# Kernel tuning notes

Hardware: AMD Instinct MI355X
Metric: run time of the kernel (lower is better)

Reference implementation:

```python
import jax, jax.numpy as jnp
import numpy as np
from jax import lax

RATIOS = (0.5, 1.0, 2.0)
SCALES = (8, 16, 32)
BASE = 16
STRIDE = 16
NMS_THRESH = 0.7
N_PRE = 6000   # n_test_pre_nms
N_POST = 300   # n_test_post_nms
MIN_SIZE = 16.0  # min_size * scale (scale=1.0)
NEG = -1e9


def _anchor_base():
    py = px = BASE / 2.0
    ab = np.zeros((len(RATIOS) * len(SCALES), 4), np.float32)
    for i, r in enumerate(RATIOS):
        for j, s in enumerate(SCALES):
            h = BASE * s * np.sqrt(r)
            w = BASE * s * np.sqrt(1.0 / r)
            k = i * len(SCALES) + j
            ab[k] = [py - h / 2.0, px - w / 2.0, py + h / 2.0, px + w / 2.0]
    return ab


def _anchors(hh, ww):
    # enumerate shifted anchors, shape [hh*ww*9, 4] in (y1,x1,y2,x2)
    ab = _anchor_base()
    sy = np.arange(hh, dtype=np.float32) * STRIDE
    sx = np.arange(ww, dtype=np.float32) * STRIDE
    sx, sy = np.meshgrid(sx, sy)
    shift = np.stack([sy.ravel(), sx.ravel(), sy.ravel(), sx.ravel()], axis=1)
    a = (ab[None, :, :] + shift[:, None, :]).reshape(-1, 4).astype(np.float32)
    return jnp.asarray(a)


def _conv(x, w, b, pad):
    y = lax.conv_general_dilated(x, w, (1, 1), [(pad, pad), (pad, pad)],
                                 dimension_numbers=('NCHW', 'OIHW', 'NCHW'))
    return y + b[None, :, None, None]


def _nms(boxes, valid):
    # greedy NMS over score-sorted boxes [N,4]; returns N_POST selected indices (-1 = pad)
    N = boxes.shape[0]
    y1, x1, y2, x2 = boxes[:, 0], boxes[:, 1], boxes[:, 2], boxes[:, 3]
    area = (y2 - y1) * (x2 - x1)
    idx = jnp.arange(N)

    def body(i, sup):
        cur = valid[i] & (~sup[i])
        ih = jnp.clip(jnp.minimum(y2[i], y2) - jnp.maximum(y1[i], y1), 0.0)
        iw = jnp.clip(jnp.minimum(x2[i], x2) - jnp.maximum(x1[i], x1), 0.0)
        inter = ih * iw
        iou = inter / (area[i] + area - inter + 1e-9)
        return sup | (cur & (iou > NMS_THRESH) & (idx > i))

    sup = lax.fori_loop(0, N, body, jnp.zeros((N,), bool))
    kept = valid & (~sup)
    rank = jnp.cumsum(kept) - 1
    sel = jnp.full((N_POST,), -1, jnp.int32)
    sel = sel.at[jnp.where(kept & (rank < N_POST), rank, N_POST)].set(
        jnp.arange(N, dtype=jnp.int32), mode='drop')
    return sel


def setup_inputs() -> dict:
    key = jax.random.key(0)
    ks = jax.random.split(key, 5)
    n, c, hh, ww = 8, 512, 64, 64
    x = jax.random.normal(ks[0], (n, c, hh, ww), jnp.float32)
    # normal_init(mean=0, std=0.01), biases zero
    w1 = 0.01 * jax.random.normal(ks[1], (512, 512, 3, 3), jnp.float32)
    b1 = jnp.zeros((512,), jnp.float32)
    w_score = 0.01 * jax.random.normal(ks[2], (18, 512, 1, 1), jnp.float32)
    b_score = jnp.zeros((18,), jnp.float32)
    w_loc = 0.01 * jax.random.normal(ks[3], (36, 512, 1, 1), jnp.float32)
    b_loc = jnp.zeros((36,), jnp.float32)
    return {"x": x, "w1": w1, "b1": b1, "w_score": w_score, "b_score": b_score,
            "w_loc": w_loc, "b_loc": b_loc, "img_h": 1024, "img_w": 1024}


def reference(x, w1, b1, w_score, b_score, w_loc, b_loc, img_h, img_w):
    n, _, hh, ww = x.shape
    anchor = _anchors(hh, ww)  # [K,4]
    mid = jax.nn.relu(_conv(x, w1, b1, 1))
    rpn_locs = _conv(mid, w_loc, b_loc, 0).transpose(0, 2, 3, 1).reshape(n, -1, 4)  # [n,K,4]
    raw = _conv(mid, w_score, b_score, 0).transpose(0, 2, 3, 1)  # [n,hh,ww,18]
    sm = jax.nn.softmax(raw.reshape(n, hh, ww, -1, 2), axis=-1)
    fg = sm[..., 1].reshape(n, -1)          # [n,K] foreground scores
    rpn_scores = raw.reshape(n, -1, 2)      # pre-softmax, as in original
    # loc2bbox decode
    ah = anchor[:, 2] - anchor[:, 0]
    aw = anchor[:, 3] - anchor[:, 1]
    acy = anchor[:, 0] + 0.5 * ah
    acx = anchor[:, 1] + 0.5 * aw
    dy, dx, dh, dw = (rpn_locs[..., 0], rpn_locs[..., 1], rpn_locs[..., 2], rpn_locs[..., 3])
    cy = dy * ah + acy
    cx = dx * aw + acx
    h = ah * jnp.exp(dh)
    w = aw * jnp.exp(dw)
    fh = jnp.float32(img_h)
    fw = jnp.float32(img_w)
    roi = jnp.stack([jnp.clip(cy - 0.5 * h, 0.0, fh), jnp.clip(cx - 0.5 * w, 0.0, fw),
                     jnp.clip(cy + 0.5 * h, 0.0, fh), jnp.clip(cx + 0.5 * w, 0.0, fw)], axis=-1)
    hs = roi[..., 2] - roi[..., 0]
    ws = roi[..., 3] - roi[..., 1]
    ok = (hs >= MIN_SIZE) & (ws >= MIN_SIZE)
    masked = jnp.where(ok, fg, NEG)
    vals, top = lax.top_k(masked, N_PRE)  # score-descending pre-NMS selection
    boxes = jnp.take_along_axis(roi, top[..., None], axis=1)  # [n,N_PRE,4]
    valid = vals > NEG / 2
    sel = jax.vmap(_nms)(boxes, valid)  # [n,N_POST]
    mask = sel >= 0
    rois = jnp.take_along_axis(boxes, jnp.clip(sel, 0)[..., None], axis=1)
    rois = jnp.where(mask[..., None], rois, 0.0)  # [n,N_POST,4], zero-padded
    roi_indices = jnp.where(mask, jnp.arange(n, dtype=jnp.int32)[:, None], -1)  # -1 = pad
    return (rpn_locs, rpn_scores, rois, roi_indices, anchor)
```

## Files before the change

kernel.cpp:

```cpp
#include <hip/hip_runtime.h>
#include <cstdint>
#include <cstddef>

#define CIN 512
#define NA 36864
#define NPRE 6000
#define NPOST 300
#define NWORD 94
#define NEGV -1000000000.0f
#define ISTRIDE 76

#define O_LOCS   0
#define O_SCORES 1179648
#define O_ROIS   1769472
#define O_RIDX   1779072
#define O_ANCH   1781472

__device__ __forceinline__ float fmulr(float a, float b) { return __fmul_rn(a, b); }
__device__ __forceinline__ float faddr(float a, float b) { return __fadd_rn(a, b); }
__device__ __forceinline__ float fsubr(float a, float b) { return __fsub_rn(a, b); }

__device__ __forceinline__ void anchor_for(int a, int pos, float* anc) {
    const double rat[3] = {0.5, 1.0, 2.0};
    const double scl[3] = {8.0, 16.0, 32.0};
    int ri = a / 3, si = a - ri * 3;
    double h = 16.0 * scl[si] * sqrt(rat[ri]);
    double w = 16.0 * scl[si] * sqrt(1.0 / rat[ri]);
    float a0 = (float)(8.0 - h * 0.5);
    float a1 = (float)(8.0 - w * 0.5);
    float a2 = (float)(8.0 + h * 0.5);
    float a3 = (float)(8.0 + w * 0.5);
    int y = pos >> 6, x = pos & 63;
    float sy = (float)(y * 16), sx = (float)(x * 16);
    anc[0] = faddr(a0, sy); anc[1] = faddr(a1, sx);
    anc[2] = faddr(a2, sy); anc[3] = faddr(a3, sx);
}

__device__ __forceinline__ bool decode_box(float4 L, const float* anc, float* box) {
    float ah  = fsubr(anc[2], anc[0]);
    float aw  = fsubr(anc[3], anc[1]);
    float acy = faddr(anc[0], fmulr(0.5f, ah));
    float acx = faddr(anc[1], fmulr(0.5f, aw));
    float cy  = faddr(fmulr(L.x, ah), acy);
    float cx  = faddr(fmulr(L.y, aw), acx);
    float h   = fmulr(ah, expf(L.z));
    float w   = fmulr(aw, expf(L.w));
    float y1 = fminf(fmaxf(fsubr(cy, fmulr(0.5f, h)), 0.0f), 1024.0f);
    float x1 = fminf(fmaxf(fsubr(cx, fmulr(0.5f, w)), 0.0f), 1024.0f);
    float y2 = fminf(fmaxf(faddr(cy, fmulr(0.5f, h)), 0.0f), 1024.0f);
    float x2 = fminf(fmaxf(faddr(cx, fmulr(0.5f, w)), 0.0f), 1024.0f);
    box[0] = y1; box[1] = x1; box[2] = y2; box[3] = x2;
    float hs = fsubr(y2, y1), ws2 = fsubr(x2, x1);
    return (hs >= 16.0f) && (ws2 >= 16.0f);
}

__device__ __forceinline__ unsigned long long mono64(double f) {
    unsigned long long u = (unsigned long long)__double_as_longlong(f);
    return (u & 0x8000000000000000ull) ? ~u : (u | 0x8000000000000000ull);
}

__global__ __launch_bounds__(256) void k_wreord(const float* __restrict__ w1,
                                                float* __restrict__ wr2) {
    __shared__ float tile[64][37];
    const int ct0 = blockIdx.x * 36;
    const int ocb = blockIdx.y;
    const int t = threadIdx.x;
    for (int i = t; i < 64 * 36; i += 256) {
        int orow = i / 36, c = i - orow * 36;
        tile[orow][c] = w1[(size_t)(ocb * 64 + orow) * 4608 + ct0 + c];
    }
    __syncthreads();
    for (int i = t; i < 36 * 64; i += 256) {
        int ct = i >> 6, o = i & 63;
        wr2[((size_t)ocb * 4608 + ct0 + ct) * 64 + o] = tile[o][ct];
    }
}

__global__ __launch_bounds__(256, 2) void k_conv3(const float* __restrict__ x,
                                                  const float* __restrict__ wr2,
                                                  const float* __restrict__ b1,
                                                  float* __restrict__ mid) {
    __shared__ float in_s[8 * 6 * ISTRIDE];
    __shared__ float w_s[8 * 9 * 64];
    const int yb  = blockIdx.x;
    const int ocb = blockIdx.y;
    const int n   = blockIdx.z;
    const int t   = threadIdx.x;
    const int y0  = yb * 4;
    const int cg  = t & 7;
    const int rg  = (t >> 3) & 1;
    const int ocg = t >> 4;
    const int xo  = cg << 3;

    if (t < 48) { in_s[t * ISTRIDE + 4] = 0.f; in_s[t * ISTRIDE + 69] = 0.f; }

    int   ilds[3];
    int   ival[3];
    const float* igp[3];
#pragma unroll
    for (int k = 0; k < 3; ++k) {
        int s = t + k * 256;
        int row = s >> 4, c = s & 15;
        int cc = row / 6, rr = row - cc * 6;
        int gy = y0 - 1 + rr;
        ival[k] = (gy >= 0 && gy < 64) ? 1 : 0;
        int gyc = min(max(gy, 0), 63);
        ilds[k] = row * ISTRIDE + 5 + c * 4;
        igp[k]  = x + (((size_t)(n * CIN + cc) * 64 + gyc) * 64 + c * 4);
    }
    const float* wgp = wr2 + (size_t)ocb * (4608 * 64);

    float acc[4][2][8];
#pragma unroll
    for (int o = 0; o < 4; o++)
#pragma unroll
        for (int rr = 0; rr < 2; rr++)
#pragma unroll
            for (int j = 0; j < 8; j++) acc[o][rr][j] = 0.f;

    for (int ch = 0; ch < 64; ++ch) {
        const float* wp0 = wgp + (size_t)ch * 4608;
#pragma unroll
        for (int k = 0; k < 4; ++k)
            *(float4*)&w_s[4 * t + 1024 * k] = *(const float4*)(wp0 + 4 * t + 1024 * k);
        if (t < 128)
            *(float4*)&w_s[4 * t + 4096] = *(const float4*)(wp0 + 4 * t + 4096);
#pragma unroll
        for (int k = 0; k < 3; ++k) {
            float4 v = make_float4(0.f, 0.f, 0.f, 0.f);
            if (ival[k]) v = *(const float4*)(igp[k] + (size_t)ch * 32768);
            in_s[ilds[k] + 0] = v.x;
            in_s[ilds[k] + 1] = v.y;
            in_s[ilds[k] + 2] = v.z;
            in_s[ilds[k] + 3] = v.w;
        }
        __syncthreads();

        float sub[4][2][8];
#pragma unroll
        for (int o = 0; o < 4; o++)
#pragma unroll
            for (int rr = 0; rr < 2; rr++)
#pragma unroll
                for (int j = 0; j < 8; j++) sub[o][rr][j] = 0.f;
#pragma unroll 1
        for (int cc = 0; cc < 8; ++cc) {
            float in4r[4][12];
#pragma unroll
            for (int k = 0; k < 4; ++k) {
                const float4* ip = (const float4*)
                    &in_s[cc * (6 * ISTRIDE) + (rg * 2 + k) * ISTRIDE + xo + 4];
                float4 A = ip[0], B = ip[1], C4 = ip[2];
                in4r[k][0] = A.x;  in4r[k][1] = A.y;  in4r[k][2]  = A.z;  in4r[k][3]  = A.w;
                in4r[k][4] = B.x;  in4r[k][5] = B.y;  in4r[k][6]  = B.z;  in4r[k][7]  = B.w;
                in4r[k][8] = C4.x; in4r[k][9] = C4.y; in4r[k][10] = C4.z; in4r[k][11] = C4.w;
            }
#pragma unroll
            for (int dy = 0; dy < 3; ++dy) {
#pragma unroll
                for (int dx = 0; dx < 3; ++dx) {
                    const float4* wp =
                        (const float4*)&w_s[cc * 576 + (dy * 3 + dx) * 64 + ocg * 4];
                    float4 W = wp[0];
                    float w4[4] = {W.x, W.y, W.z, W.w};
#pragma unroll
                    for (int o = 0; o < 4; ++o)
#pragma unroll
                        for (int rr = 0; rr < 2; ++rr)
#pragma unroll
                            for (int j = 0; j < 8; ++j)
                                sub[o][rr][j] += w4[o] * in4r[rr + dy][j + dx];
                }
            }
        }
#pragma unroll
        for (int o = 0; o < 4; o++)
#pragma unroll
            for (int rr = 0; rr < 2; rr++)
#pragma unroll
                for (int j = 0; j < 8; j++) acc[o][rr][j] += sub[o][rr][j];
        __syncthreads();
    }
    const int ocbase = (ocb << 6) + ocg * 4;
#pragma unroll
    for (int o = 0; o < 4; o++) {
        float bb = b1[ocbase + o];
#pragma unroll
        for (int rr = 0; rr < 2; rr++) {
            const int gy = y0 + rg * 2 + rr;
            float4 v0, v1;
            v0.x = fmaxf(acc[o][rr][0] + bb, 0.f);
            v0.y = fmaxf(acc[o][rr][1] + bb, 0.f);
            v0.z = fmaxf(acc[o][rr][2] + bb, 0.f);
            v0.w = fmaxf(acc[o][rr][3] + bb, 0.f);
            v1.x = fmaxf(acc[o][rr][4] + bb, 0.f);
            v1.y = fmaxf(acc[o][rr][5] + bb, 0.f);
            v1.z = fmaxf(acc[o][rr][6] + bb, 0.f);
            v1.w = fmaxf(acc[o][rr][7] + bb, 0.f);
            float* mp = &mid[((size_t)(n * CIN + ocbase + o) * 64 + gy) * 64 + xo];
            *(float4*)(mp + 0) = v0;
            *(float4*)(mp + 4) = v1;
        }
    }
}

__global__ __launch_bounds__(256) void k_conv1(const float* __restrict__ mid,
                                               const float* __restrict__ wl,
                                               const float* __restrict__ bl,
                                               const float* __restrict__ wsc,
                                               const float* __restrict__ bs,
                                               float* __restrict__ out,
                                               double* __restrict__ fgbuf) {
    __shared__ float in_s[128 * 64];
    __shared__ float w_s[128 * 64];
    const int y = blockIdx.x;
    const int n = blockIdx.y;
    const int t = threadIdx.x;
    const int xx = t & 63, og = t >> 6;
    double accd[14];
#pragma unroll
    for (int k = 0; k < 14; k++) accd[k] = 0.0;

    for (int c0 = 0; c0 < 512; c0 += 128) {
        for (int idx = t; idx < 128 * 64; idx += 256) {
            int cc = idx >> 6, x2 = idx & 63;
            in_s[idx] = mid[((n * CIN + c0 + cc) * 64 + y) * 64 + x2];
        }
        for (int idx = t; idx < 128 * 64; idx += 256) {
            int cc = idx >> 6, s = idx & 63;
            int og2 = s >> 4, kk = s & 15;
            int oc = og2 * 14 + kk;
            float v = 0.f;
            if (kk < 14 && oc < 54)
                v = (oc < 36) ? wl[oc * 512 + c0 + cc] : wsc[(oc - 36) * 512 + c0 + cc];
            w_s[cc * 64 + s] = v;
        }
        __syncthreads();
#pragma unroll 1
        for (int cc = 0; cc < 128; ++cc) {
            double iv = (double)in_s[cc * 64 + xx];
            const float4* wq = (const float4*)&w_s[cc * 64 + og * 16];
            float4 W0 = wq[0], W1 = wq[1], W2 = wq[2], W3 = wq[3];
            float wf[16] = {W0.x, W0.y, W0.z, W0.w, W1.x, W1.y, W1.z, W1.w,
                            W2.x, W2.y, W2.z, W2.w, W3.x, W3.y, W3.z, W3.w};
#pragma unroll
            for (int k = 0; k < 14; k++)
                accd[k] += (double)wf[k] * iv;
        }
        __syncthreads();
    }
    const int pos = y * 64 + xx;
    double sv[14];
#pragma unroll
    for (int k = 0; k < 14; k++) {
        int oc = og * 14 + k;
        if (oc >= 54) break;
        if (oc < 36) {
            double v = accd[k] + (double)bl[oc];
            int a = oc >> 2, cd = oc & 3;
            out[O_LOCS + ((size_t)(n * NA + pos * 9 + a)) * 4 + cd] = (float)v;
        } else {
            sv[k] = accd[k] + (double)bs[oc - 36];
            int c2 = oc - 36, a = c2 >> 1, cls = c2 & 1;
            out[O_SCORES + ((size_t)(n * NA + pos * 9 + a)) * 2 + cls] = (float)sv[k];
        }
    }
#pragma unroll
    for (int k = 0; k < 13; k++) {
        int oc = og * 14 + k;
        if (oc >= 36 && oc < 54 && ((oc - 36) & 1) == 0) {
            double s0 = sv[k], s1 = sv[k + 1];
            double m = fmax(s0, s1);
            double e0 = exp(s0 - m), e1 = exp(s1 - m);
            double fg = e1 / (e0 + e1);
            int a = (oc - 36) >> 1;
            fgbuf[(size_t)n * NA + pos * 9 + a] = fg;
        }
    }
}

__global__ __launch_bounds__(256) void k_keys(const float* __restrict__ out_ro,
                                              const double* __restrict__ fgbuf,
                                              unsigned long long* __restrict__ keys,
                                              float* __restrict__ out) {
    const int n = blockIdx.x / 144;
    const int i = (blockIdx.x % 144) * 256 + threadIdx.x;
    int pos = i / 9, a = i - pos * 9;
    float anc[4]; anchor_for(a, pos, anc);
    float4 L = *(const float4*)&out_ro[O_LOCS + (size_t)(n * NA + i) * 4];
    float box[4];
    bool ok = decode_box(L, anc, box);
    double f = ok ? fgbuf[(size_t)n * NA + i] : (double)NEGV;
    unsigned long long m = mono64(f);
    keys[(size_t)n * NA + i] =
        (m & 0xFFFFFFFFFFFF0000ull) | (unsigned long long)(0xFFFFu - (unsigned)i);
    if (blockIdx.x < 144) {
        out[O_ANCH + (size_t)i * 4 + 0] = anc[0];
        out[O_ANCH + (size_t)i * 4 + 1] = anc[1];
        out[O_ANCH + (size_t)i * 4 + 2] = anc[2];
        out[O_ANCH + (size_t)i * 4 + 3] = anc[3];
    }
}

__global__ __launch_bounds__(1024) void k_select(const unsigned long long* __restrict__ keys,
                                                 unsigned long long* __restrict__ kth,
                                                 unsigned int* __restrict__ cnt) {
    __shared__ unsigned int hist[8192];
    __shared__ unsigned int gs[256];
    __shared__ unsigned int s_rem, s_G;
    __shared__ unsigned long long s_pref;
    const int n = blockIdx.x, t = threadIdx.x;
    if (t == 0) { s_rem = NPRE; s_pref = 0ull; }
    __syncthreads();
    const int shifts[5] = {51, 38, 25, 12, 0};
    const int widths[5] = {13, 13, 13, 13, 12};
    int plen = 0;
    for (int lev = 0; lev < 5; ++lev) {
        const int nb = 1 << widths[lev];
        const int gsz = nb >> 8;
        for (int b = t; b < nb; b += 1024) hist[b] = 0;
        __syncthreads();
        const unsigned long long pref = s_pref;
        for (int i = t; i < NA; i += 1024) {
            unsigned long long key = keys[(size_t)n * NA + i];
            if (plen == 0 || (key >> (64 - plen)) == pref) {
                unsigned int bin = (unsigned int)((key >> shifts[lev]) & (unsigned)(nb - 1));
                atomicAdd(&hist[bin], 1u);
            }
        }
        __syncthreads();
        if (t < 256) {
            unsigned int s = 0;
            for (int m = 0; m < gsz; m++) s += hist[t * gsz + m];
            gs[t] = s;
        }
        __syncthreads();
        for (int off = 1; off < 256; off <<= 1) {
            unsigned int v = 0;
            if (t < 256 && t + off < 256) v = gs[t + off];
            __syncthreads();
            if (t < 256) gs[t] += v;
            __syncthreads();
        }
        const unsigned int rem = s_rem;
        if (t < 256) {
            unsigned int here = gs[t];
            unsigned int above = (t == 255) ? 0u : gs[t + 1];
            if (here >= rem && above < rem) s_G = (unsigned int)t;
        }
        __syncthreads();
        if (t == 0) {
            int G = (int)s_G;
            unsigned int acc = (G == 255) ? 0u : gs[G + 1];
            int selbin = G * gsz;
            for (int b = G * gsz + gsz - 1; b >= G * gsz; --b) {
                if (acc + hist[b] >= rem) { selbin = b; break; }
                acc += hist[b];
            }
            s_rem = rem - acc;
            s_pref = (s_pref << widths[lev]) | (unsigned long long)(unsigned)selbin;
        }
        plen += widths[lev];
        __syncthreads();
    }
    if (t == 0) { kth[n] = s_pref; cnt[n] = 0u; }
}

__global__ void k_compact(const unsigned long long* __restrict__ keys,
                          const unsigned long long* __restrict__ kth,
                          unsigned long long* __restrict__ cbuf,
                          unsigned int* __restrict__ cnt) {
    const int n = blockIdx.x / 144;
    const int i = (blockIdx.x % 144) * 256 + threadIdx.x;
    unsigned long long key = keys[(size_t)n * NA + i];
    if (key >= kth[n]) {
        unsigned int p = atomicAdd(&cnt[n], 1u);
        if (p < 8192) cbuf[(size_t)n * 8192 + p] = key;
    }
}

__global__ __launch_bounds__(256) void k_rank(const unsigned long long* __restrict__ cbuf,
                                              const float* __restrict__ out,
                                              float* __restrict__ bsort,
                                              unsigned char* __restrict__ vflag) {
    __shared__ unsigned long long tile[2048];
    const int n = blockIdx.y, t = threadIdx.x;
    const int base = blockIdx.x * 512;
    unsigned long long mykey[2]; int myrank[2]; bool have[2];
#pragma unroll
    for (int m = 0; m < 2; ++m) {
        int idx = base + t * 2 + m;
        have[m] = idx < NPRE;
        mykey[m] = have[m] ? cbuf[(size_t)n * 8192 + idx] : 0ull;
        myrank[m] = 0;
    }
    for (int tb = 0; tb < 3; ++tb) {
        for (int jj = t; jj < 2048; jj += 256) {
            int j = tb * 2048 + jj;
            tile[jj] = (j < NPRE) ? cbuf[(size_t)n * 8192 + j] : 0ull;
        }
        __syncthreads();
        const int jmax = min(2048, NPRE - tb * 2048);
        for (int j = 0; j < jmax; ++j) {
            unsigned long long kj = tile[j];
            if (kj > mykey[0]) myrank[0]++;
            if (kj > mykey[1]) myrank[1]++;
        }
        __syncthreads();
    }
#pragma unroll
    for (int m = 0; m < 2; ++m) {
        if (!have[m]) continue;
        unsigned long long key = mykey[m];
        unsigned int i = 0xFFFFu - (unsigned int)(key & 0xFFFFull);
        int pos = i / 9, a = i - pos * 9;
        float anc[4]; anchor_for(a, pos, anc);
        float4 L = *(const float4*)&out[O_LOCS + (size_t)(n * NA + i) * 4];
        float box[4];
        bool ok = decode_box(L, anc, box);
        ((float4*)bsort)[(size_t)n * NPRE + myrank[m]] =
            make_float4(box[0], box[1], box[2], box[3]);
        vflag[(size_t)n * NPRE + myrank[m]] = ok ? 1 : 0;
    }
}

__global__ __launch_bounds__(256) void k_mask(const float* __restrict__ bsort,
                                              unsigned long long* __restrict__ masks) {
    __shared__ float4 bx[1024];
    const int n  = blockIdx.z;
    const int jc = blockIdx.y;
    const int i  = blockIdx.x * 256 + threadIdx.x;
    const bool have = i < NPRE;
    float4 bi = make_float4(0, 0, 0, 0); float areai = 0.f;
    if (have) {
        bi = ((const float4*)bsort)[(size_t)n * NPRE + i];
        areai = fmulr(fsubr(bi.z, bi.x), fsubr(bi.w, bi.y));
    }
    const int jn = min(1024, NPRE - jc * 1024);
    for (int jj = threadIdx.x; jj < jn; jj += 256)
        bx[jj] = ((const float4*)bsort)[(size_t)n * NPRE + jc * 1024 + jj];
    __syncthreads();
    for (int w = 0; w < 16; ++w) {
        int gw = jc * 16 + w;
        if (gw >= NWORD) break;
        unsigned long long m = 0ull;
        int jbase = jc * 1024 + w * 64;
        if (have && jbase + 63 > i) {
#pragma unroll 1
            for (int b = 0; b < 64; b++) {
                int j = jbase + b;
                if (j > i && j < NPRE) {
                    float4 bj = bx[w * 64 + b];
                    float ih = fmaxf(fsubr(fminf(bi.z, bj.z), fmaxf(bi.x, bj.x)), 0.f);
                    float iw = fmaxf(fsubr(fminf(bi.w, bj.w), fmaxf(bi.y, bj.y)), 0.f);
                    float inter = fmulr(ih, iw);
                    float areaj = fmulr(fsubr(bj.z, bj.x), fsubr(bj.w, bj.y));
                    float den = faddr(fsubr(faddr(areai, areaj), inter), 1e-9f);
                    float iou = __fdiv_rn(inter, den);
                    if (iou > 0.7f) m |= (1ull << b);
                }
            }
        }
        if (have) masks[((size_t)n * NPRE + i) * NWORD + gw] = m;
    }
}

__global__ __launch_bounds__(64) void k_scan(const unsigned long long* __restrict__ masks,
                                             const unsigned char* __restrict__ vflag,
                                             const float* __restrict__ bsort,
                                             float* __restrict__ out) {
    const int n = blockIdx.x;
    const int l = threadIdx.x;
    unsigned long long valw0 = 0ull, valw1 = 0ull;
    for (int w = 0; w < NWORD; ++w) {
        int idx = w * 64 + l;
        bool v = (idx < NPRE) && (vflag[(size_t)n * NPRE + idx] != 0);
        unsigned long long word = __ballot(v);
        if (w == l) valw0 = word;
        if (w == 64 + l) valw1 = word;
    }
    unsigned long long sup0 = 0ull, sup1 = 0ull;
    int kept = 0;
    while (kept < NPOST) {
        unsigned long long cand0 = valw0 & ~sup0;
        unsigned long long cand1 = (l < NWORD - 64) ? (valw1 & ~sup1) : 0ull;
        unsigned long long b0 = __ballot(cand0 != 0ull);
        int w; unsigned long long bits;
        if (b0) {
            int fl = __ffsll((long long)b0) - 1;
            w = fl; bits = __shfl(cand0, fl);
        } else {
            unsigned long long b1 = __ballot(cand1 != 0ull);
            if (!b1) break;
            int fl = __ffsll((long long)b1) - 1;
            w = 64 + fl; bits = __shfl(cand1, fl);
        }
        int i = w * 64 + (__ffsll((long long)bits) - 1);
        if (l == 0) {
            float4 b4 = ((const float4*)bsort)[(size_t)n * NPRE + i];
            out[O_ROIS + (size_t)(n * NPOST + kept) * 4 + 0] = b4.x;
            out[O_ROIS + (size_t)(n * NPOST + kept) * 4 + 1] = b4.y;
            out[O_ROIS + (size_t)(n * NPOST + kept) * 4 + 2] = b4.z;
            out[O_ROIS + (size_t)(n * NPOST + kept) * 4 + 3] = b4.w;
            out[O_RIDX + n * NPOST + kept] = (float)n;
        }
        kept++;
        if (kept >= NPOST) break;
        const unsigned long long* mrow = masks + ((size_t)n * NPRE + i) * NWORD;
        sup0 |= mrow[l];
        if (l < NWORD - 64) sup1 |= mrow[64 + l];
        if (w < 64) { if (l == w) sup0 |= (1ull << (i & 63)); }
        else        { if (l == w - 64) sup1 |= (1ull << (i & 63)); }
    }
    for (int r = kept + l; r < NPOST; r += 64) {
        out[O_ROIS + (size_t)(n * NPOST + r) * 4 + 0] = 0.f;
        out[O_ROIS + (size_t)(n * NPOST + r) * 4 + 1] = 0.f;
        out[O_ROIS + (size_t)(n * NPOST + r) * 4 + 2] = 0.f;
        out[O_ROIS + (size_t)(n * NPOST + r) * 4 + 3] = 0.f;
        out[O_RIDX + n * NPOST + r] = -1.0f;
    }
}

extern "C" void kernel_launch(void* const* d_in, const int* in_sizes, int n_in,
                              void* d_out, int out_size, void* d_ws, size_t ws_size,
                              hipStream_t stream) {
    const float* x   = (const float*)d_in[0];
    const float* w1  = (const float*)d_in[1];
    const float* b1  = (const float*)d_in[2];
    const float* wsc = (const float*)d_in[3];
    const float* bsc = (const float*)d_in[4];
    const float* wlc = (const float*)d_in[5];
    const float* blc = (const float*)d_in[6];
    float* out = (float*)d_out;
    char* ws = (char*)d_ws;

    float* wr2                = (float*)(ws + 0);
    float* mid                = (float*)(ws + 9437184);
    double* fgbuf             = (double*)(ws + 76546048);
    unsigned long long* keys  = (unsigned long long*)(ws + 78905344);
    unsigned long long* kth   = (unsigned long long*)(ws + 81264640);
    unsigned int* cnt         = (unsigned int*)(ws + 81265152);
    unsigned long long* cbuf  = (unsigned long long*)(ws + 81265664);
    float* bsort              = (float*)(ws + 81789952);
    unsigned char* vflag      = (unsigned char*)(ws + 82557952);
    unsigned long long* masks = (unsigned long long*)(ws + 82606080);

    dim3 gw(128, 8);
    k_wreord<<<gw, 256, 0, stream>>>(w1, wr2);
    dim3 g3(16, 8, 8);
    k_conv3<<<g3, 256, 0, stream>>>(x, wr2, b1, mid);
    dim3 g1(64, 8);
    k_conv1<<<g1, 256, 0, stream>>>(mid, wlc, blc, wsc, bsc, out, fgbuf);
    k_keys<<<1152, 256, 0, stream>>>(out, fgbuf, keys, out);
    k_select<<<8, 1024, 0, stream>>>(keys, kth, cnt);
    k_compact<<<1152, 256, 0, stream>>>(keys, kth, cbuf, cnt);
    dim3 gr(12, 8);
    k_rank<<<gr, 256, 0, stream>>>(cbuf, out, bsort, vflag);
    dim3 gm(24, 6, 8);
    k_mask<<<gm, 256, 0, stream>>>(bsort, masks);
    k_scan<<<8, 64, 0, stream>>>(masks, vflag, bsort, out);
}
```

Before: 2.590 ms.

## Fuse top-k select, compact and rank into one kernel; restructure conv3 inner loop

The radix select, compaction and rank kernels are merged into one per-image 1024-thread kernel. It compacts the selected keys into shared memory and ranks them there, which removes two launches and the global cbuf round trip. Separately, the conv3 inner loop now loads input rows incrementally per dy to lower register pressure, and its launch bound is raised to 3 blocks per CU. The cost is that ranking now runs on only 8 blocks, each doing 6000x6 comparisons per thread, instead of 96 blocks. The tighter register cap on conv3 could cause spills.

Result: slower. 3.784 ms (+46.1%).

```diff
diff --git a/kernel.cpp b/kernel.cpp
--- a/kernel.cpp
+++ b/kernel.cpp
@@ -76,7 +76,7 @@
     }
 }
 
-__global__ __launch_bounds__(256, 2) void k_conv3(const float* __restrict__ x,
+__global__ __launch_bounds__(256, 3) void k_conv3(const float* __restrict__ x,
                                                   const float* __restrict__ wr2,
                                                   const float* __restrict__ b1,
                                                   float* __restrict__ mid) {
@@ -145,33 +145,44 @@
                 for (int j = 0; j < 8; j++) sub[o][rr][j] = 0.f;
 #pragma unroll 1
         for (int cc = 0; cc < 8; ++cc) {
-            float in4r[4][12];
-#pragma unroll
-            for (int k = 0; k < 4; ++k) {
-                const float4* ip = (const float4*)
-                    &in_s[cc * (6 * ISTRIDE) + (rg * 2 + k) * ISTRIDE + xo + 4];
-                float4 A = ip[0], B = ip[1], C4 = ip[2];
-                in4r[k][0] = A.x;  in4r[k][1] = A.y;  in4r[k][2]  = A.z;  in4r[k][3]  = A.w;
-                in4r[k][4] = B.x;  in4r[k][5] = B.y;  in4r[k][6]  = B.z;  in4r[k][7]  = B.w;
-                in4r[k][8] = C4.x; in4r[k][9] = C4.y; in4r[k][10] = C4.z; in4r[k][11] = C4.w;
+            const float* rowbase = &in_s[cc * (6 * ISTRIDE) + xo + 4];
+            float r0[12], r1[12], r2[12], r3[12];
+#define LOADROW(dst, K)                                                        \
+            {                                                                  \
+                const float4* ip = (const float4*)(rowbase + (rg * 2 + (K)) * ISTRIDE); \
+                float4 A = ip[0], B = ip[1], C4 = ip[2];                       \
+                dst[0] = A.x;  dst[1] = A.y;  dst[2]  = A.z;  dst[3]  = A.w;   \
+                dst[4] = B.x;  dst[5] = B.y;  dst[6]  = B.z;  dst[7]  = B.w;   \
+                dst[8] = C4.x; dst[9] = C4.y; dst[10] = C4.z; dst[11] = C4.w;  \
             }
-#pragma unroll
-            for (int dy = 0; dy < 3; ++dy) {
-#pragma unroll
-                for (int dx = 0; dx < 3; ++dx) {
-                    const float4* wp =
-                        (const float4*)&w_s[cc * 576 + (dy * 3 + dx) * 64 + ocg * 4];
-                    float4 W = wp[0];
-                    float w4[4] = {W.x, W.y, W.z, W.w};
-#pragma unroll
-                    for (int o = 0; o < 4; ++o)
-#pragma unroll
-                        for (int rr = 0; rr < 2; ++rr)
-#pragma unroll
-                            for (int j = 0; j < 8; ++j)
-                                sub[o][rr][j] += w4[o] * in4r[rr + dy][j + dx];
-                }
+#define MACDY(DY, RA, RB)                                                      \
+            {                                                                  \
+                _Pragma("unroll")                                              \
+                for (int dx = 0; dx < 3; ++dx) {                               \
+                    const float4* wp =                                         \
+                        (const float4*)&w_s[cc * 576 + ((DY) * 3 + dx) * 64 + ocg * 4]; \
+                    float4 W = wp[0];                                          \
+                    float w4[4] = {W.x, W.y, W.z, W.w};                        \
+                    _Pragma("unroll")                                          \
+                    for (int o = 0; o < 4; ++o) {                              \
+                        _Pragma("unroll")                                      \
+                        for (int j = 0; j < 8; ++j)                            \
+                            sub[o][0][j] += w4[o] * RA[j + dx];                \
+                        _Pragma("unroll")                                      \
+                        for (int j = 0; j < 8; ++j)                            \
+                            sub[o][1][j] += w4[o] * RB[j + dx];                \
+                    }                                                          \
+                }                                                              \
             }
+            LOADROW(r0, 0)
+            LOADROW(r1, 1)
+            MACDY(0, r0, r1)
+            LOADROW(r2, 2)
+            MACDY(1, r1, r2)
+            LOADROW(r3, 3)
+            MACDY(2, r2, r3)
+#undef LOADROW
+#undef MACDY
         }
 #pragma unroll
         for (int o = 0; o < 4; o++)
@@ -302,13 +313,16 @@
     }
 }
 
-__global__ __launch_bounds__(1024) void k_select(const unsigned long long* __restrict__ keys,
-                                                 unsigned long long* __restrict__ kth,
-                                                 unsigned int* __restrict__ cnt) {
-    __shared__ unsigned int hist[8192];
-    __shared__ unsigned int gs[256];
-    __shared__ unsigned int s_rem, s_G;
-    __shared__ unsigned long long s_pref;
+__global__ __launch_bounds__(1024) void k_topk(const unsigned long long* __restrict__ keys,
+                                               const float* __restrict__ out,
+                                               float* __restrict__ bsort,
+                                               unsigned char* __restrict__ vflag) {
+    __shared__ union U {
+        struct { unsigned int hist[8192]; unsigned int gs[256]; } sel;
+        unsigned long long arr[6016];
+    } sm;
+    __shared__ unsigned long long s_pref, s_kth;
+    __shared__ unsigned int s_rem, s_G, s_cnt;
     const int n = blockIdx.x, t = threadIdx.x;
     if (t == 0) { s_rem = NPRE; s_pref = 0ull; }
     __syncthreads();
@@ -318,44 +332,44 @@
     for (int lev = 0; lev < 5; ++lev) {
         const int nb = 1 << widths[lev];
         const int gsz = nb >> 8;
-        for (int b = t; b < nb; b += 1024) hist[b] = 0;
+        for (int b = t; b < nb; b += 1024) sm.sel.hist[b] = 0;
         __syncthreads();
         const unsigned long long pref = s_pref;
         for (int i = t; i < NA; i += 1024) {
             unsigned long long key = keys[(size_t)n * NA + i];
             if (plen == 0 || (key >> (64 - plen)) == pref) {
                 unsigned int bin = (unsigned int)((key >> shifts[lev]) & (unsigned)(nb - 1));
-                atomicAdd(&hist[bin], 1u);
+                atomicAdd(&sm.sel.hist[bin], 1u);
             }
         }
         __syncthreads();
         if (t < 256) {
             unsigned int s = 0;
-            for (int m = 0; m < gsz; m++) s += hist[t * gsz + m];
-            gs[t] = s;
+            for (int m = 0; m < gsz; m++) s += sm.sel.hist[t * gsz + m];
+            sm.sel.gs[t] = s;
         }
         __syncthreads();
         for (int off = 1; off < 256; off <<= 1) {
             unsigned int v = 0;
-            if (t < 256 && t + off < 256) v = gs[t + off];
+            if (t < 256 && t + off < 256) v = sm.sel.gs[t + off];
             __syncthreads();
-            if (t < 256) gs[t] += v;
+            if (t < 256) sm.sel.gs[t] += v;
             __syncthreads();
         }
         const unsigned int rem = s_rem;
         if (t < 256) {
-            unsigned int here = gs[t];
-            unsigned int above = (t == 255) ? 0u : gs[t + 1];
+            unsigned int here = sm.sel.gs[t];
+            unsigned int above = (t == 255) ? 0u : sm.sel.gs[t + 1];
             if (here >= rem && above < rem) s_G = (unsigned int)t;
         }
         __syncthreads();
         if (t == 0) {
             int G = (int)s_G;
-            unsigned int acc = (G == 255) ? 0u : gs[G + 1];
+            unsigned int acc = (G == 255) ? 0u : sm.sel.gs[G + 1];
             int selbin = G * gsz;
             for (int b = G * gsz + gsz - 1; b >= G * gsz; --b) {
-                if (acc + hist[b] >= rem) { selbin = b; break; }
-                acc += hist[b];
+                if (acc + sm.sel.hist[b] >= rem) { selbin = b; break; }
+                acc += sm.sel.hist[b];
             }
             s_rem = rem - acc;
             s_pref = (s_pref << widths[lev]) | (unsigned long long)(unsigned)selbin;
@@ -363,64 +377,45 @@
         plen += widths[lev];
         __syncthreads();
     }
-    if (t == 0) { kth[n] = s_pref; cnt[n] = 0u; }
-}
-
-__global__ void k_compact(const unsigned long long* __restrict__ keys,
-                          const unsigned long long* __restrict__ kth,
-                          unsigned long long* __restrict__ cbuf,
-                          unsigned int* __restrict__ cnt) {
-    const int n = blockIdx.x / 144;
-    const int i = (blockIdx.x % 144) * 256 + threadIdx.x;
-    unsigned long long key = keys[(size_t)n * NA + i];
-    if (key >= kth[n]) {
-        unsigned int p = atomicAdd(&cnt[n], 1u);
-        if (p < 8192) cbuf[(size_t)n * 8192 + p] = key;
-    }
-}
-
-__global__ __launch_bounds__(256) void k_rank(const unsigned long long* __restrict__ cbuf,
-                                              const float* __restrict__ out,
-                                              float* __restrict__ bsort,
-                                              unsigned char* __restrict__ vflag) {
-    __shared__ unsigned long long tile[2048];
-    const int n = blockIdx.y, t = threadIdx.x;
-    const int base = blockIdx.x * 512;
-    unsigned long long mykey[2]; int myrank[2]; bool have[2];
-#pragma unroll
-    for (int m = 0; m < 2; ++m) {
-        int idx = base + t * 2 + m;
-        have[m] = idx < NPRE;
-        mykey[m] = have[m] ? cbuf[(size_t)n * 8192 + idx] : 0ull;
-        myrank[m] = 0;
-    }
-    for (int tb = 0; tb < 3; ++tb) {
-        for (int jj = t; jj < 2048; jj += 256) {
-            int j = tb * 2048 + jj;
-            tile[jj] = (j < NPRE) ? cbuf[(size_t)n * 8192 + j] : 0ull;
-        }
-        __syncthreads();
-        const int jmax = min(2048, NPRE - tb * 2048);
-        for (int j = 0; j < jmax; ++j) {
-            unsigned long long kj = tile[j];
-            if (kj > mykey[0]) myrank[0]++;
-            if (kj > mykey[1]) myrank[1]++;
-        }
-        __syncthreads();
-    }
-#pragma unroll
-    for (int m = 0; m < 2; ++m) {
-        if (!have[m]) continue;
-        unsigned long long key = mykey[m];
+    if (t == 0) { s_kth = s_pref; s_cnt = 0u; }
+    __syncthreads();
+    const unsigned long long kth = s_kth;
+    for (int i = t; i < NA; i += 1024) {
+        unsigned long long key = keys[(size_t)n * NA + i];
+        if (key >= kth) {
+            unsigned int p = atomicAdd(&s_cnt, 1u);
+            if (p < 6016) sm.arr[p] = key;
+        }
+    }
+    __syncthreads();
+    unsigned long long myk[6];
+    int myr[6];
+#pragma unroll
+    for (int m = 0; m < 6; ++m) {
+        int idx = t + m * 1024;
+        myk[m] = (idx < NPRE) ? sm.arr[idx] : 0xFFFFFFFFFFFFFFFFull;
+        myr[m] = 0;
+    }
+#pragma unroll 4
+    for (int j = 0; j < NPRE; ++j) {
+        unsigned long long kj = sm.arr[j];
+#pragma unroll
+        for (int m = 0; m < 6; ++m) myr[m] += (kj > myk[m]) ? 1 : 0;
+    }
+#pragma unroll
+    for (int m = 0; m < 6; ++m) {
+        int idx = t + m * 1024;
+        if (idx >= NPRE) continue;
+        unsigned long long key = myk[m];
         unsigned int i = 0xFFFFu - (unsigned int)(key & 0xFFFFull);
         int pos = i / 9, a = i - pos * 9;
         float anc[4]; anchor_for(a, pos, anc);
         float4 L = *(const float4*)&out[O_LOCS + (size_t)(n * NA + i) * 4];
         float box[4];
         bool ok = decode_box(L, anc, box);
-        ((float4*)bsort)[(size_t)n * NPRE + myrank[m]] =
+        ((float4*)bsort)[(size_t)n * NPRE + myr[m]] =
             make_float4(box[0], box[1], box[2], box[3]);
-        vflag[(size_t)n * NPRE + myrank[m]] = ok ? 1 : 0;
+        vflag[(size_t)n * NPRE + myr[m]] = ok ? 1 : 0;
     }
 }
 
@@ -538,9 +533,6 @@
     float* mid                = (float*)(ws + 9437184);
     double* fgbuf             = (double*)(ws + 76546048);
     unsigned long long* keys  = (unsigned long long*)(ws + 78905344);
-    unsigned long long* kth   = (unsigned long long*)(ws + 81264640);
-    unsigned int* cnt         = (unsigned int*)(ws + 81265152);
-    unsigned long long* cbuf  = (unsigned long long*)(ws + 81265664);
     float* bsort              = (float*)(ws + 81789952);
     unsigned char* vflag      = (unsigned char*)(ws + 82557952);
     unsigned long long* masks = (unsigned long long*)(ws + 82606080);
@@ -552,10 +544,7 @@
     dim3 g1(64, 8);
     k_conv1<<<g1, 256, 0, stream>>>(mid, wlc, blc, wsc, bsc, out, fgbuf);
     k_keys<<<1152, 256, 0, stream>>>(out, fgbuf, keys, out);
-    k_select<<<8, 1024, 0, stream>>>(keys, kth, cnt);
-    k_compact<<<1152, 256, 0, stream>>>(keys, kth, cbuf, cnt);
-    dim3 gr(12, 8);
-    k_rank<<<gr, 256, 0, stream>>>(cbuf, out, bsort, vflag);
+    k_topk<<<8, 1024, 0, stream>>>(keys, out, bsort, vflag);
     dim3 gm(24, 6, 8);
     k_mask<<<gm, 256, 0, stream>>>(bsort, masks);
     k_scan<<<8, 64, 0, stream>>>(masks, vflag, bsort, out);
```
